# Kernel tuning notes

Hardware: AMD Instinct MI355X
Metric: run time of the kernel (lower is better)

## Reference

```python
import jax, jax.numpy as jnp
import numpy as np

L = 16384      # sequence length
D_IN = 512     # d_input
D_H = 1024     # d_hidden
D_OUT = 512    # d_output
R_MIN = 0.0
R_MAX = 0.99
MAX_PHASE = np.pi


def setup_inputs() -> dict:
    key = jax.random.key(0)
    k_nu, k_th, k_x, k_bre, k_bim, k_cre, k_cim, k_d = jax.random.split(key, 8)
    # nu_init with parametrization='exp'
    u_nu = jax.random.uniform(k_nu, (D_H,), dtype=jnp.float32)
    nu = jnp.sqrt(u_nu * (R_MAX ** 2 - R_MIN ** 2) + R_MIN ** 2)
    u_theta = jax.random.uniform(k_th, (D_H,), dtype=jnp.float32, minval=-MAX_PHASE, maxval=MAX_PHASE)
    theta = jnp.mod(u_theta, 2 * jnp.pi)
    lamb = jnp.stack([jnp.log(-jnp.log(nu)), jnp.log(theta)], axis=0)  # [2, D_H]
    # gamma_init with parametrization='exp': nu = exp(-exp(lamb[0]))
    nu_eff = jnp.exp(-jnp.exp(lamb[0]))
    gamma = jnp.log(jnp.sqrt(1.0 - jnp.abs(nu_eff) ** 2))  # [D_H]
    # matrix_init: normal / sqrt(shape[0])
    B_re = jax.random.normal(k_bre, (D_H, D_IN), dtype=jnp.float32) / jnp.sqrt(D_H)
    B_im = jax.random.normal(k_bim, (D_H, D_IN), dtype=jnp.float32) / jnp.sqrt(D_H)
    C_re = jax.random.normal(k_cre, (D_OUT, D_H), dtype=jnp.float32) / jnp.sqrt(D_OUT)
    C_im = jax.random.normal(k_cim, (D_OUT, D_H), dtype=jnp.float32) / jnp.sqrt(D_OUT)
    D = jax.random.normal(k_d, (D_OUT, D_IN), dtype=jnp.float32) / jnp.sqrt(D_OUT)
    inputs = jax.random.normal(k_x, (L, D_IN), dtype=jnp.float32)
    return {"inputs": inputs, "lamb": lamb, "gamma": gamma,
            "B_re": B_re, "B_im": B_im, "C_re": C_re, "C_im": C_im, "D": D}


def _binary_operator_diag(q_i, q_j):
    A_i, b_i = q_i
    A_j, b_j = q_j
    return (A_j * A_i, A_j * b_i + b_j)


def reference(inputs, lamb, gamma, B_re, B_im, C_re, C_im, D):
    # parametrization='exp': lambda = exp(-exp(nu_log) + i*exp(theta_log))
    diag_lambda = jnp.exp(-jnp.exp(lamb[0]) + 1j * jnp.exp(lamb[1]))  # [D_H] complex64
    # which_gamma='learned', exp param: scale rows of B by exp(gamma)
    B_norm = jnp.exp(gamma)[:, None] * (B_re + 1j * B_im)             # [D_H, D_IN]
    # Bu_t = B_norm @ x_t for all t, as one GEMM: [L, D_H] complex
    Bu = inputs.astype(B_norm.dtype) @ B_norm.T
    Lambda_elements = jnp.broadcast_to(diag_lambda[None, :], Bu.shape)
    # diagonal linear recurrence h_t = lambda*h_{t-1} + Bu_t via parallel scan
    _, h = jax.lax.associative_scan(_binary_operator_diag, (Lambda_elements, Bu))
    C = C_re + 1j * C_im
    # y_t = Re[C h_t] + D x_t
    outputs = jnp.real(h @ C.T) + inputs @ D.T  # [L, D_OUT]
    return outputs
```

## Files before the change

kernel.cpp:

```cpp
#include <hip/hip_runtime.h>

__device__ __forceinline__ unsigned short f2b(float f) {
    unsigned int u = __builtin_bit_cast(unsigned int, f);
    unsigned int r = (u + 0x7FFFu + ((u >> 16) & 1u)) >> 16;
    return (unsigned short)r;
}
__device__ __forceinline__ float b2f(unsigned short s) {
    unsigned int u = ((unsigned int)s) << 16;
    return __builtin_bit_cast(float, u);
}

typedef __attribute__((ext_vector_type(8))) short short8;
typedef __attribute__((ext_vector_type(4))) float float4v;

#define GLD16(g, l) __builtin_amdgcn_global_load_lds(                          \
    (const __attribute__((address_space(1))) unsigned int*)(g),                \
    (__attribute__((address_space(3))) unsigned int*)(l), 16, 0, 0)

#define SEQLEN 16384
#define NCHUNK 512
#define TCHUNK 32
#define LDH 2560

__global__ void prep_all(const float* __restrict__ x,
                         const float* __restrict__ B_re, const float* __restrict__ B_im,
                         const float* __restrict__ gamma,
                         const float* __restrict__ C_re, const float* __restrict__ C_im,
                         const float* __restrict__ Dm,
                         unsigned short* __restrict__ Hcat,
                         unsigned short* __restrict__ Bcat,
                         unsigned short* __restrict__ CW) {
    int b = blockIdx.x;
    if (b < 8192) {
        int id = b * 256 + threadIdx.x;
        int t = id >> 7;
        int k4 = (id & 127) << 2;
        float4 v = *(const float4*)(x + (long)t * 512 + k4);
        ushort4 o;
        o.x = f2b(v.x); o.y = f2b(v.y); o.z = f2b(v.z); o.w = f2b(v.w);
        *(ushort4*)(Hcat + (long)t * LDH + 2048 + k4) = o;
    } else if (b < 9216) {
        int id = (b - 8192) * 256 + threadIdx.x;
        int n = id >> 7;
        int k4 = (id & 127) << 2;
        const float* src = (n < 1024) ? (B_re + (long)n * 512) : (B_im + (long)(n - 1024) * 512);
        float g = expf(gamma[n & 1023]);
        float4 v = *(const float4*)(src + k4);
        ushort4 o;
        o.x = f2b(v.x * g); o.y = f2b(v.y * g); o.z = f2b(v.z * g); o.w = f2b(v.w * g);
        *(ushort4*)(Bcat + (long)n * 512 + k4) = o;
    } else {
        int id = (b - 9216) * 256 + threadIdx.x;
        int o = id / 640;
        int j4 = (id - o * 640) << 2;
        float4 v; float sgn = 1.0f;
        if (j4 < 1024) {
            v = *(const float4*)(C_re + (long)o * 1024 + j4);
        } else if (j4 < 2048) {
            v = *(const float4*)(C_im + (long)o * 1024 + (j4 - 1024));
            sgn = -1.0f;
        } else {
            v = *(const float4*)(Dm + (long)o * 512 + (j4 - 2048));
        }
        ushort4 w;
        w.x = f2b(v.x * sgn); w.y = f2b(v.y * sgn); w.z = f2b(v.z * sgn); w.w = f2b(v.w * sgn);
        *(ushort4*)(CW + (long)o * 2560 + j4) = w;
    }
}

template <bool OUT_BF16>
__launch_bounds__(256)
__global__ void gemm_bt(const unsigned short* __restrict__ A, int lda,
                        const unsigned short* __restrict__ B, int ldb,
                        void* __restrict__ Cout, int ldc, int Ktot,
                        int nbx_shift, int nby_d8) {
    __shared__ unsigned short As[128 * 32] __attribute__((aligned(16)));
    __shared__ unsigned short Bs[128 * 32] __attribute__((aligned(16)));
    const int tid = threadIdx.x;
    const int wave = tid >> 6;
    const int lane = tid & 63;

    const int bid = blockIdx.x;
    const int xcd = bid & 7;
    const int g = bid >> 3;
    const int bx = g & ((1 << nbx_shift) - 1);
    const int by = xcd * nby_d8 + (g >> nbx_shift);
    const long m0 = (long)by * 128;
    const long n0 = (long)bx * 128;

    const int wm = (wave >> 1) * 64;
    const int wn = (wave & 1) * 64;

    const int s1 = wave * 64 + lane;
    const int r1 = s1 >> 2, c1 = (s1 & 3) * 8;
    const int s2 = s1 + 256;
    const int r2 = s2 >> 2, c2 = (s2 & 3) * 8;
    const unsigned short* Arow1 = A + (m0 + r1) * lda + c1;
    const unsigned short* Arow2 = A + (m0 + r2) * lda + c2;
    const unsigned short* Brow1 = B + (n0 + r1) * ldb + c1;
    const unsigned short* Brow2 = B + (n0 + r2) * ldb + c2;
    char* AsB1 = (char*)As + wave * 1024;
    char* AsB2 = (char*)As + 4096 + wave * 1024;
    char* BsB1 = (char*)Bs + wave * 1024;
    char* BsB2 = (char*)Bs + 4096 + wave * 1024;

    const int fr = lane & 15;
    const int fk = (lane >> 4) * 8;

    float4v acc[4][4] = {};

    for (int k0 = 0; k0 < Ktot; k0 += 32) {
        GLD16(Arow1 + k0, AsB1);
        GLD16(Arow2 + k0, AsB2);
        GLD16(Brow1 + k0, BsB1);
        GLD16(Brow2 + k0, BsB2);
        __syncthreads();
        short8 af[4], bfr[4];
#pragma unroll
        for (int i = 0; i < 4; i++) {
            af[i]  = *(const short8*)(As + (wm + i * 16 + fr) * 32 + fk);
            bfr[i] = *(const short8*)(Bs + (wn + i * 16 + fr) * 32 + fk);
        }
#pragma unroll
        for (int mi = 0; mi < 4; mi++)
#pragma unroll
            for (int ni = 0; ni < 4; ni++)
                acc[mi][ni] = __builtin_amdgcn_mfma_f32_16x16x32_bf16(af[mi], bfr[ni], acc[mi][ni], 0, 0, 0);
        __syncthreads();
    }

    const int er = (lane >> 4) * 4;
    const int ec = lane & 15;
#pragma unroll
    for (int mi = 0; mi < 4; mi++) {
#pragma unroll
        for (int r = 0; r < 4; r++) {
            long grow = m0 + wm + mi * 16 + er + r;
#pragma unroll
            for (int ni = 0; ni < 4; ni++) {
                long gcol = n0 + wn + ni * 16 + ec;
                float v = acc[mi][ni][r];
                if (OUT_BF16)
                    ((unsigned short*)Cout)[grow * ldc + gcol] = f2b(v);
                else
                    ((float*)Cout)[grow * ldc + gcol] = v;
            }
        }
    }
}

__global__ void scan_ends(const unsigned short* __restrict__ Hcat,
                          const float* __restrict__ lamb,
                          float* __restrict__ E) {
    const int chunk = blockIdx.x;
    const int ch = threadIdx.x << 2;
    float lre[4], lim[4];
#pragma unroll
    for (int i = 0; i < 4; i++) {
        float nu = expf(-expf(lamb[ch + i]));
        float th = expf(lamb[1024 + ch + i]);
        lre[i] = nu * cosf(th);
        lim[i] = nu * sinf(th);
    }
    float hr[4] = {0, 0, 0, 0}, hi[4] = {0, 0, 0, 0};
    const unsigned short* base = Hcat + (long)chunk * TCHUNK * LDH + ch;
#pragma unroll 4
    for (int t = 0; t < TCHUNK; t++) {
        ushort4 br = *(const ushort4*)(base + (long)t * LDH);
        ushort4 bi = *(const ushort4*)(base + (long)t * LDH + 1024);
        float brf[4] = {b2f(br.x), b2f(br.y), b2f(br.z), b2f(br.w)};
        float bif[4] = {b2f(bi.x), b2f(bi.y), b2f(bi.z), b2f(bi.w)};
#pragma unroll
        for (int i = 0; i < 4; i++) {
            float nr = fmaf(lre[i], hr[i], fmaf(-lim[i], hi[i], brf[i]));
            float ni = fmaf(lre[i], hi[i], fmaf(lim[i], hr[i], bif[i]));
            hr[i] = nr; hi[i] = ni;
        }
    }
    float* Ec = E + (long)chunk * 2048 + ch;
#pragma unroll
    for (int i = 0; i < 4; i++) {
        Ec[i] = hr[i];
        Ec[1024 + i] = hi[i];
    }
}

__global__ void carry(const float* __restrict__ lamb, const float* __restrict__ E,
                      float* __restrict__ Kc) {
    const int ch = blockIdx.x * 256 + threadIdx.x;
    double nu = exp(-exp((double)lamb[ch]));
    double th = exp((double)lamb[1024 + ch]);
    double lr = nu * cos(th), li = nu * sin(th);
#pragma unroll
    for (int i = 0; i < 5; i++) {
        double rr = lr * lr - li * li;
        double ii = 2.0 * lr * li;
        lr = rr; li = ii;
    }
    float tre = (float)lr, tim = (float)li;
    float hr = 0.0f, hi = 0.0f;
#pragma unroll 8
    for (int c = 0; c < NCHUNK; c++) {
        Kc[(long)c * 2048 + ch] = hr;
        Kc[(long)c * 2048 + 1024 + ch] = hi;
        float er = E[(long)c * 2048 + ch];
        float ei = E[(long)c * 2048 + 1024 + ch];
        float nr = fmaf(tre, hr, fmaf(-tim, hi, er));
        float ni = fmaf(tre, hi, fmaf(tim, hr, ei));
        hr = nr; hi = ni;
    }
}

__global__ void scan_apply(unsigned short* __restrict__ Hcat,
                           const float* __restrict__ lamb,
                           const float* __restrict__ Kc) {
    const int chunk = blockIdx.x;
    const int ch = threadIdx.x << 2;
    float lre[4], lim[4];
#pragma unroll
    for (int i = 0; i < 4; i++) {
        float nu = expf(-expf(lamb[ch + i]));
        float th = expf(lamb[1024 + ch + i]);
        lre[i] = nu * cosf(th);
        lim[i] = nu * sinf(th);
    }
    float hr[4], hi[4];
#pragma unroll
    for (int i = 0; i < 4; i++) {
        hr[i] = Kc[(long)chunk * 2048 + ch + i];
        hi[i] = Kc[(long)chunk * 2048 + 1024 + ch + i];
    }
    unsigned short* base = Hcat + (long)chunk * TCHUNK * LDH + ch;
#pragma unroll 4
    for (int t = 0; t < TCHUNK; t++) {
        ushort4 br = *(const ushort4*)(base + (long)t * LDH);
        ushort4 bi = *(const ushort4*)(base + (long)t * LDH + 1024);
        float brf[4] = {b2f(br.x), b2f(br.y), b2f(br.z), b2f(br.w)};
        float bif[4] = {b2f(bi.x), b2f(bi.y), b2f(bi.z), b2f(bi.w)};
#pragma unroll
        for (int i = 0; i < 4; i++) {
            float nr = fmaf(lre[i], hr[i], fmaf(-lim[i], hi[i], brf[i]));
            float ni = fmaf(lre[i], hi[i], fmaf(lim[i], hr[i], bif[i]));
            hr[i] = nr; hi[i] = ni;
        }
        ushort4 orv, oiv;
        orv.x = f2b(hr[0]); orv.y = f2b(hr[1]); orv.z = f2b(hr[2]); orv.w = f2b(hr[3]);
        oiv.x = f2b(hi[0]); oiv.y = f2b(hi[1]); oiv.z = f2b(hi[2]); oiv.w = f2b(hi[3]);
        *(ushort4*)(base + (long)t * LDH) = orv;
        *(ushort4*)(base + (long)t * LDH + 1024) = oiv;
    }
}

extern "C" void kernel_launch(void* const* d_in, const int* in_sizes, int n_in,
                              void* d_out, int out_size, void* d_ws, size_t ws_size,
                              hipStream_t stream) {
    const float* x     = (const float*)d_in[0];
    const float* lamb  = (const float*)d_in[1];
    const float* gamma = (const float*)d_in[2];
    const float* B_re  = (const float*)d_in[3];
    const float* B_im  = (const float*)d_in[4];
    const float* C_re  = (const float*)d_in[5];
    const float* C_im  = (const float*)d_in[6];
    const float* Dm    = (const float*)d_in[7];

    char* ws = (char*)d_ws;
    unsigned short* Hcat = (unsigned short*)ws;
    float* E  = (float*)(ws + 83886080);
    float* Kc = E + (long)NCHUNK * 2048;
    unsigned short* Bcat = (unsigned short*)((char*)Kc + 4194304);
    unsigned short* CW   = Bcat + (long)2048 * 512;

    prep_all<<<10496, 256, 0, stream>>>(x, B_re, B_im, gamma, C_re, C_im, Dm, Hcat, Bcat, CW);
    gemm_bt<true><<<2048, 256, 0, stream>>>(Hcat + 2048, LDH, Bcat, 512, Hcat, LDH, 512,
                                            4, 16);
    scan_ends<<<NCHUNK, 256, 0, stream>>>(Hcat, lamb, E);
    carry<<<4, 256, 0, stream>>>(lamb, E, Kc);
    scan_apply<<<NCHUNK, 256, 0, stream>>>(Hcat, lamb, Kc);
    gemm_bt<false><<<512, 256, 0, stream>>>(Hcat, LDH, CW, 2560, d_out, 512, 2560,
                                            2, 16);
}
```

Baseline: 290.3 us.

## Stage bf16 GEMM epilogue through LDS and halve output tile width for final GEMM

The first GEMM now writes its bf16 results into shared memory and copies them out as 16-byte vector stores, replacing scattered 2-byte global writes. The final GEMM, which has K=2560 and only 512 blocks, is split into a specialized kernel with 128x64 tiles, doubling the block count to 1024 for better CU occupancy. The cost is extra LDS traffic and barriers in the epilogue, and lower reuse of A in the final GEMM because each A tile is now loaded by twice as many blocks.

Result: no change. 293.0 us (+0.9%).

```diff
diff --git a/kernel.cpp b/kernel.cpp
--- a/kernel.cpp
+++ b/kernel.cpp
@@ -68,14 +68,14 @@
     }
 }
 
-template <bool OUT_BF16>
 __launch_bounds__(256)
-__global__ void gemm_bt(const unsigned short* __restrict__ A, int lda,
-                        const unsigned short* __restrict__ B, int ldb,
-                        void* __restrict__ Cout, int ldc, int Ktot,
-                        int nbx_shift, int nby_d8) {
-    __shared__ unsigned short As[128 * 32] __attribute__((aligned(16)));
-    __shared__ unsigned short Bs[128 * 32] __attribute__((aligned(16)));
+__global__ void gemm_bf16out(const unsigned short* __restrict__ A, int lda,
+                             const unsigned short* __restrict__ B, int ldb,
+                             unsigned short* __restrict__ Cout, int ldc, int Ktot,
+                             int nbx_shift, int nby_d8) {
+    __shared__ unsigned short smem[8192] __attribute__((aligned(16)));
+    unsigned short* As = smem;
+    unsigned short* Bs = smem + 4096;
     const int tid = threadIdx.x;
     const int wave = tid >> 6;
     const int lane = tid & 63;
@@ -131,20 +131,96 @@
 
     const int er = (lane >> 4) * 4;
     const int ec = lane & 15;
+    const int rowg = wm >> 6;
+#pragma unroll
+    for (int mi = 0; mi < 4; mi++) {
+        __syncthreads();
+#pragma unroll
+        for (int ni = 0; ni < 4; ni++)
+#pragma unroll
+            for (int r = 0; r < 4; r++)
+                smem[(rowg * 16 + er + r) * 136 + wn + ni * 16 + ec] = f2b(acc[mi][ni][r]);
+        __syncthreads();
+#pragma unroll
+        for (int h = 0; h < 2; h++) {
+            int j = h * 256 + tid;
+            int rp = j >> 4;
+            int cp = (j & 15) * 8;
+            short8 v = *(const short8*)(smem + rp * 136 + cp);
+            long grow = m0 + (rp >> 4) * 64 + mi * 16 + (rp & 15);
+            *(short8*)(Cout + grow * ldc + n0 + cp) = v;
+        }
+    }
+}
+
+__launch_bounds__(256)
+__global__ void gemm_f32out(const unsigned short* __restrict__ A, int lda,
+                            const unsigned short* __restrict__ B, int ldb,
+                            float* __restrict__ Cout, int ldc, int Ktot) {
+    __shared__ unsigned short smem[6144] __attribute__((aligned(16)));
+    unsigned short* As = smem;
+    unsigned short* Bs = smem + 4096;
+    const int tid = threadIdx.x;
+    const int wave = tid >> 6;
+    const int lane = tid & 63;
+
+    const int bid = blockIdx.x;
+    const int xcd = bid & 7;
+    const int g = bid >> 3;
+    const int bx = g & 7;
+    const int by = xcd * 16 + (g >> 3);
+    const long m0 = (long)by * 128;
+    const long n0 = (long)bx * 64;
+
+    const int wm = (wave >> 1) * 64;
+    const int wn = (wave & 1) * 32;
+
+    const int s1 = wave * 64 + lane;
+    const int r1 = s1 >> 2, c1 = (s1 & 3) * 8;
+    const int s2 = s1 + 256;
+    const int r2 = s2 >> 2, c2 = (s2 & 3) * 8;
+    const unsigned short* Arow1 = A + (m0 + r1) * lda + c1;
+    const unsigned short* Arow2 = A + (m0 + r2) * lda + c2;
+    const unsigned short* Brow1 = B + (n0 + r1) * ldb + c1;
+    char* AsB1 = (char*)As + wave * 1024;
+    char* AsB2 = (char*)As + 4096 + wave * 1024;
+    char* BsB1 = (char*)Bs + wave * 1024;
+
+    const int fr = lane & 15;
+    const int fk = (lane >> 4) * 8;
+
+    float4v acc[4][2] = {};
+
+    for (int k0 = 0; k0 < Ktot; k0 += 32) {
+        GLD16(Arow1 + k0, AsB1);
+        GLD16(Arow2 + k0, AsB2);
+        GLD16(Brow1 + k0, BsB1);
+        __syncthreads();
+        short8 af[4], bfr[2];
+#pragma unroll
+        for (int i = 0; i < 4; i++)
+            af[i] = *(const short8*)(As + (wm + i * 16 + fr) * 32 + fk);
+#pragma unroll
+        for (int i = 0; i < 2; i++)
+            bfr[i] = *(const short8*)(Bs + (wn + i * 16 + fr) * 32 + fk);
+#pragma unroll
+        for (int mi = 0; mi < 4; mi++)
+#pragma unroll
+            for (int ni = 0; ni < 2; ni++)
+                acc[mi][ni] = __builtin_amdgcn_mfma_f32_16x16x32_bf16(af[mi], bfr[ni], acc[mi][ni], 0, 0, 0);
+        __syncthreads();
+    }
+
+    const int er = (lane >> 4) * 4;
+    const int ec = lane & 15;
 #pragma unroll
     for (int mi = 0; mi < 4; mi++) {
 #pragma unroll
         for (int r = 0; r < 4; r++) {
             long grow = m0 + wm + mi * 16 + er + r;
 #pragma unroll
-            for (int ni = 0; ni < 4; ni++) {
-                long gcol = n0 + wn + ni * 16 + ec;
-                float v = acc[mi][ni][r];
-                if (OUT_BF16)
-                    ((unsigned short*)Cout)[grow * ldc + gcol] = f2b(v);
-                else
-                    ((float*)Cout)[grow * ldc + gcol] = v;
-            }
+            for (int ni = 0; ni < 2; ni++)
+                Cout[grow * ldc + n0 + wn + ni * 16 + ec] = acc[mi][ni][r];
         }
     }
 }
@@ -271,11 +347,10 @@
     unsigned short* CW   = Bcat + (long)2048 * 512;
 
     prep_all<<<10496, 256, 0, stream>>>(x, B_re, B_im, gamma, C_re, C_im, Dm, Hcat, Bcat, CW);
-    gemm_bt<true><<<2048, 256, 0, stream>>>(Hcat + 2048, LDH, Bcat, 512, Hcat, LDH, 512,
-                                            4, 16);
+    gemm_bf16out<<<2048, 256, 0, stream>>>(Hcat + 2048, LDH, Bcat, 512, Hcat, LDH, 512,
+                                           4, 16);
     scan_ends<<<NCHUNK, 256, 0, stream>>>(Hcat, lamb, E);
     carry<<<4, 256, 0, stream>>>(lamb, E, Kc);
     scan_apply<<<NCHUNK, 256, 0, stream>>>(Hcat, lamb, Kc);
-    gemm_bt<false><<<512, 256, 0, stream>>>(Hcat, LDH, CW, 2560, d_out, 512, 2560,
-                                            2, 16);
-}
+    gemm_f32out<<<1024, 256, 0, stream>>>(Hcat, LDH, CW, 2560, (float*)d_out, 512, 2560);
+}
```

## Replace 4-wave GEMM with single-wave 64x128 tile kernel using double-buffered LDS

Applied to the files above, without the earlier changes.

Rewrites both GEMMs to use one 64-thread wave per block computing a 64x128 tile. Global-to-LDS loads go into a two-stage shared buffer, with s_waitcnt on vmcnt replacing __syncthreads. The goal is to overlap the next K-slice load with the MFMA work and to drop block-level barriers. The cost is a smaller per-block tile with more blocks, a larger accumulator register footprint per wave, and lower reuse of A/B per block.

Measured after the change: 293.6 us. No clear change (+1.2%).

```diff
diff --git a/kernel.cpp b/kernel.cpp
--- a/kernel.cpp
+++ b/kernel.cpp
@@ -69,65 +69,64 @@
 }
 
 template <bool OUT_BF16>
-__launch_bounds__(256)
-__global__ void gemm_bt(const unsigned short* __restrict__ A, int lda,
-                        const unsigned short* __restrict__ B, int ldb,
-                        void* __restrict__ Cout, int ldc, int Ktot,
-                        int nbx_shift, int nby_d8) {
-    __shared__ unsigned short As[128 * 32] __attribute__((aligned(16)));
-    __shared__ unsigned short Bs[128 * 32] __attribute__((aligned(16)));
-    const int tid = threadIdx.x;
-    const int wave = tid >> 6;
-    const int lane = tid & 63;
+__launch_bounds__(64, 2)
+__global__ void gemm_w64(const unsigned short* __restrict__ A, int lda,
+                         const unsigned short* __restrict__ B, int ldb,
+                         void* __restrict__ Cout, int ldc, int Ktot,
+                         int nbx_shift) {
+    __shared__ unsigned short sm[2][6144] __attribute__((aligned(16)));
+    const int lane = threadIdx.x;
 
     const int bid = blockIdx.x;
     const int xcd = bid & 7;
     const int g = bid >> 3;
     const int bx = g & ((1 << nbx_shift) - 1);
-    const int by = xcd * nby_d8 + (g >> nbx_shift);
-    const long m0 = (long)by * 128;
+    const int by = xcd * 32 + (g >> nbx_shift);
+    const long m0 = (long)by * 64;
     const long n0 = (long)bx * 128;
 
-    const int wm = (wave >> 1) * 64;
-    const int wn = (wave & 1) * 64;
-
-    const int s1 = wave * 64 + lane;
-    const int r1 = s1 >> 2, c1 = (s1 & 3) * 8;
-    const int s2 = s1 + 256;
-    const int r2 = s2 >> 2, c2 = (s2 & 3) * 8;
-    const unsigned short* Arow1 = A + (m0 + r1) * lda + c1;
-    const unsigned short* Arow2 = A + (m0 + r2) * lda + c2;
-    const unsigned short* Brow1 = B + (n0 + r1) * ldb + c1;
-    const unsigned short* Brow2 = B + (n0 + r2) * ldb + c2;
-    char* AsB1 = (char*)As + wave * 1024;
-    char* AsB2 = (char*)As + 4096 + wave * 1024;
-    char* BsB1 = (char*)Bs + wave * 1024;
-    char* BsB2 = (char*)Bs + 4096 + wave * 1024;
+    const unsigned short* Ag = A + (m0 + (lane >> 2)) * lda + (lane & 3) * 8;
+    const unsigned short* Bg = B + (n0 + (lane >> 2)) * ldb + (lane & 3) * 8;
 
     const int fr = lane & 15;
     const int fk = (lane >> 4) * 8;
 
-    float4v acc[4][4] = {};
-
-    for (int k0 = 0; k0 < Ktot; k0 += 32) {
-        GLD16(Arow1 + k0, AsB1);
-        GLD16(Arow2 + k0, AsB2);
-        GLD16(Brow1 + k0, BsB1);
-        GLD16(Brow2 + k0, BsB2);
-        __syncthreads();
-        short8 af[4], bfr[4];
-#pragma unroll
-        for (int i = 0; i < 4; i++) {
-            af[i]  = *(const short8*)(As + (wm + i * 16 + fr) * 32 + fk);
-            bfr[i] = *(const short8*)(Bs + (wn + i * 16 + fr) * 32 + fk);
-        }
+    float4v acc[4][8] = {};
+
+    auto stage = [&](int b, int k0) {
+#pragma unroll
+        for (int i = 0; i < 4; i++)
+            GLD16(Ag + (long)i * 16 * lda + k0, &sm[b][i * 512]);
+#pragma unroll
+        for (int j = 0; j < 8; j++)
+            GLD16(Bg + (long)j * 16 * ldb + k0, &sm[b][2048 + j * 512]);
+    };
+    auto compute = [&](int b) {
+        short8 af[4], bf8[8];
+#pragma unroll
+        for (int i = 0; i < 4; i++)
+            af[i] = *(const short8*)(&sm[b][(i * 16 + fr) * 32 + fk]);
+#pragma unroll
+        for (int j = 0; j < 8; j++)
+            bf8[j] = *(const short8*)(&sm[b][2048 + (j * 16 + fr) * 32 + fk]);
 #pragma unroll
         for (int mi = 0; mi < 4; mi++)
 #pragma unroll
-            for (int ni = 0; ni < 4; ni++)
-                acc[mi][ni] = __builtin_amdgcn_mfma_f32_16x16x32_bf16(af[mi], bfr[ni], acc[mi][ni], 0, 0, 0);
-        __syncthreads();
-    }
+            for (int ni = 0; ni < 8; ni++)
+                acc[mi][ni] = __builtin_amdgcn_mfma_f32_16x16x32_bf16(af[mi], bf8[ni], acc[mi][ni], 0, 0, 0);
+    };
+
+    stage(0, 0);
+    int buf = 0;
+    int k0 = 0;
+    for (; k0 + 32 < Ktot; k0 += 32) {
+        stage(buf ^ 1, k0 + 32);
+        __builtin_amdgcn_s_waitcnt(0x0F7C);
+        compute(buf);
+        buf ^= 1;
+    }
+    __builtin_amdgcn_s_waitcnt(0x0F70);
+    compute(buf);
 
     const int er = (lane >> 4) * 4;
     const int ec = lane & 15;
@@ -135,10 +134,10 @@
     for (int mi = 0; mi < 4; mi++) {
 #pragma unroll
         for (int r = 0; r < 4; r++) {
-            long grow = m0 + wm + mi * 16 + er + r;
-#pragma unroll
-            for (int ni = 0; ni < 4; ni++) {
-                long gcol = n0 + wn + ni * 16 + ec;
+            long grow = m0 + mi * 16 + er + r;
+#pragma unroll
+            for (int ni = 0; ni < 8; ni++) {
+                long gcol = n0 + ni * 16 + ec;
                 float v = acc[mi][ni][r];
                 if (OUT_BF16)
                     ((unsigned short*)Cout)[grow * ldc + gcol] = f2b(v);
@@ -271,11 +270,11 @@
     unsigned short* CW   = Bcat + (long)2048 * 512;
 
     prep_all<<<10496, 256, 0, stream>>>(x, B_re, B_im, gamma, C_re, C_im, Dm, Hcat, Bcat, CW);
-    gemm_bt<true><<<2048, 256, 0, stream>>>(Hcat + 2048, LDH, Bcat, 512, Hcat, LDH, 512,
-                                            4, 16);
+    gemm_w64<true><<<4096, 64, 0, stream>>>(Hcat + 2048, LDH, Bcat, 512, Hcat, LDH, 512,
+                                            4);
     scan_ends<<<NCHUNK, 256, 0, stream>>>(Hcat, lamb, E);
     carry<<<4, 256, 0, stream>>>(lamb, E, Kc);
     scan_apply<<<NCHUNK, 256, 0, stream>>>(Hcat, lamb, Kc);
-    gemm_bt<false><<<512, 256, 0, stream>>>(Hcat, LDH, CW, 2560, d_out, 512, 2560,
-                                            2, 16);
-}
+    gemm_w64<false><<<1024, 64, 0, stream>>>(Hcat, LDH, CW, 2560, (float*)d_out, 512, 2560,
+                                             2);
+}
```
